# Kernel optimization log

Measured on AMD Instinct MI355X. Metric: run time of the kernel, lower is better.

Reference implementation:

```python
import jax, jax.numpy as jnp
import numpy as np

NF = 64            # n_filter
CFAC = 3           # SinSobel c_factor: identity + sobel-x + sobel-y
FIN = NF * CFAC    # dyna block input channels (192)
FH = NF * 2        # dyna hidden (128)
FOUT = NF          # dyna output (64)
LAT = 512
N_CALLS = 6        # ceil(log2(128) - log2(2))
P_SIZES = [FH * FIN, FH, FH * FH, FH, FOUT * FH, FOUT, FOUT * FIN, FOUT]
P_TOTAL = sum(P_SIZES)  # 61824
_OFFS = np.cumsum([0] + P_SIZES)

def act(t):
    return jax.nn.leaky_relu(t, 0.2)

def conv1x1(x, w, b):
    # x [B,I,H,W], w [O,I] -> [B,O,H,W]
    return jnp.einsum('bihw,oi->bohw', x, w) + b[None, :, None, None]

def res_block(x, w0, b0, w1, b1):
    # GAN-stability style residual block with 1x1 convs
    return x + 0.1 * conv1x1(act(conv1x1(act(x), w0, b0)), w1, b1)

def depthwise3x3(x, k2d):
    C = x.shape[1]
    k = jnp.broadcast_to(k2d.astype(x.dtype), (C, 1, 3, 3))
    return jax.lax.conv_general_dilated(
        x, k, (1, 1), [(1, 1), (1, 1)],
        dimension_numbers=('NCHW', 'OIHW', 'NCHW'),
        feature_group_count=C)

SOBEL_X = jnp.array([[1., 0., -1.], [2., 0., -2.], [1., 0., -1.]], jnp.float32) / 8.0
SOBEL_Y = SOBEL_X.T
_g = jnp.exp(-0.5 * jnp.array([-1., 0., 1.], jnp.float32) ** 2)
GAUSS = jnp.outer(_g, _g)
GAUSS = GAUSS / GAUSS.sum()

def sin_sobel(x):
    return jnp.concatenate([x, depthwise3x3(x, SOBEL_X), depthwise3x3(x, SOBEL_Y)], axis=1)

def dyna_residual(x, params):
    # per-sample hypernetwork-generated 1x1-conv residual block
    B = x.shape[0]
    def take(i, shape):
        return params[:, _OFFS[i]:_OFFS[i + 1]].reshape((B,) + shape)
    w_in, b_in = take(0, (FH, FIN)), take(1, (FH,))
    w_mid, b_mid = take(2, (FH, FH)), take(3, (FH,))
    w_out, b_out = take(4, (FOUT, FH)), take(5, (FOUT,))
    w_sk, b_sk = take(6, (FOUT, FIN)), take(7, (FOUT,))
    def pconv(h, w, b):  # batched per-sample 1x1 conv
        return jnp.einsum('bihw,boi->bohw', h, w) + b[:, :, None, None]
    x_s = pconv(x, w_sk, b_sk)
    dx = pconv(x, w_in, b_in)
    dx = pconv(act(dx), w_mid, b_mid)
    dx = pconv(act(dx), w_out, b_out)
    return x_s + dx

def downsample(x):
    # GaussianSmoothing(k=3, sigma=1, pad=1) then bilinear 0.5
    # (align_corners=False bilinear at scale 0.5 == 2x2 average pooling)
    x = depthwise3x3(x, GAUSS)
    B, C, H, W = x.shape
    return x.reshape(B, C, H // 2, 2, W // 2, 2).mean(axis=(3, 5))

def lin_res(x, w1, b1, w2, b2, sw=None, sb=None):
    x_s = x if sw is None else x @ sw + sb
    return x_s + 0.1 * (act(act(x) @ w1 + b1) @ w2 + b2)

def forward(x, inj_lat, leak, in_w, in_b, inrb_w0, inrb_b0, inrb_w1, inrb_b1,
            hyp_w, hyp_b, outrb_w0, outrb_b0, outrb_w1, outrb_b1,
            l1_sw, l1_sb, l1_w1, l1_b1, l1_w2, l1_b2,
            l2_w1, l2_b1, l2_w2, l2_b2, lo_w, lo_b):
    out = conv1x1(x, in_w, in_b)
    out = res_block(out, inrb_w0, inrb_b0, inrb_w1, inrb_b1)
    leak_f = jnp.clip(leak, 0.001, 1000.0)
    dyn_params = inj_lat @ hyp_w + hyp_b  # [B, P_TOTAL], shared across calls
    out_embs = [out]
    for _ in range(N_CALLS):  # fixed small layer loop; spatial dims halve each call
        out_new = sin_sobel(out)
        out_new = dyna_residual(out_new, dyn_params)
        out = out + leak_f * out_new
        out = downsample(out)
        out_embs.append(out)
    out = res_block(out, outrb_w0, outrb_b0, outrb_w1, outrb_b1)
    h = out.mean(axis=(2, 3))  # [B, NF]
    h = lin_res(h, l1_w1, l1_b1, l1_w2, l1_b2, l1_sw, l1_sb)
    h = lin_res(h, l2_w1, l2_b1, l2_w2, l2_b2)
    lat = h @ lo_w + lo_b
    return lat, out_embs

def setup_inputs() -> dict:
    key = jax.random.key(0)
    ks = jax.random.split(key, 24)
    B, C, S = 8, 3, 128
    def rn(k, shape, scale=0.05):
        return scale * jax.random.normal(k, shape, jnp.float32)
    z = lambda n: jnp.zeros((n,), jnp.float32)
    return {
        'x': jax.random.normal(ks[0], (B, C, S, S), jnp.float32),
        'inj_lat': jax.random.normal(ks[1], (B, LAT), jnp.float32),
        'leak': jnp.array(0.1, jnp.float32),
        'in_w': rn(ks[2], (NF, C)), 'in_b': z(NF),
        'inrb_w0': rn(ks[3], (NF, NF)), 'inrb_b0': z(NF),
        'inrb_w1': rn(ks[4], (NF, NF)), 'inrb_b1': z(NF),
        'hyp_w': rn(ks[5], (LAT, P_TOTAL), 0.01), 'hyp_b': rn(ks[6], (P_TOTAL,), 0.01),
        'outrb_w0': rn(ks[7], (NF, NF)), 'outrb_b0': z(NF),
        'outrb_w1': rn(ks[8], (NF, NF)), 'outrb_b1': z(NF),
        'l1_sw': rn(ks[9], (NF, LAT)), 'l1_sb': z(LAT),
        'l1_w1': rn(ks[10], (NF, 2 * LAT)), 'l1_b1': z(2 * LAT),
        'l1_w2': rn(ks[11], (2 * LAT, LAT)), 'l1_b2': z(LAT),
        'l2_w1': rn(ks[12], (LAT, LAT)), 'l2_b1': z(LAT),
        'l2_w2': rn(ks[13], (LAT, LAT)), 'l2_b2': z(LAT),
        'lo_w': rn(ks[14], (LAT, LAT)), 'lo_b': z(LAT),
    }

def reference(x, inj_lat, leak, in_w, in_b, inrb_w0, inrb_b0, inrb_w1, inrb_b1,
              hyp_w, hyp_b, outrb_w0, outrb_b0, outrb_w1, outrb_b1,
              l1_sw, l1_sb, l1_w1, l1_b1, l1_w2, l1_b2,
              l2_w1, l2_b1, l2_w2, l2_b2, lo_w, lo_b):
    lat, out_embs = forward(x, inj_lat, leak, in_w, in_b, inrb_w0, inrb_b0, inrb_w1, inrb_b1,
                            hyp_w, hyp_b, outrb_w0, outrb_b0, outrb_w1, outrb_b1,
                            l1_sw, l1_sb, l1_w1, l1_b1, l1_w2, l1_b2,
                            l2_w1, l2_b1, l2_w2, l2_b2, lo_w, lo_b)
    return (lat, *out_embs)
```

## Files before the change

kernel.cpp:

```cpp
#include <hip/hip_runtime.h>


#define BATCH 8
#define PT 61824

typedef __attribute__((ext_vector_type(8))) short bf16x8;
typedef __attribute__((ext_vector_type(4))) float f32x4;

__device__ __forceinline__ float lrelu(float v) { return v > 0.f ? v : 0.2f * v; }

__device__ __forceinline__ short f2bf(float f) {
    union { float fv; unsigned u; } v; v.fv = f;
    return (short)((v.u + 0x7fffu + ((v.u >> 16) & 1u)) >> 16);
}

__global__ __launch_bounds__(256) void hyper_kernel(
    const float* __restrict__ inj, const float* __restrict__ hw,
    const float* __restrict__ hb, float* __restrict__ dyn,
    short* __restrict__ dyn16)
{
    __shared__ float s_l[512 * 8];
    int t = threadIdx.x;
    for (int i = t; i < 4096; i += 256) {
        int b = i >> 9, k = i & 511;
        s_l[k * 8 + b] = inj[i];
    }
    __syncthreads();
    int p = blockIdx.x * 256 + t;
    if (p >= PT) return;
    float acc[8];
#pragma unroll
    for (int b = 0; b < 8; ++b) acc[b] = 0.f;
    for (int k = 0; k < 512; ++k) {
        float w = hw[(size_t)k * PT + p];
        float4 a0 = *(const float4*)&s_l[k * 8];
        float4 a1 = *(const float4*)&s_l[k * 8 + 4];
        acc[0] += a0.x * w; acc[1] += a0.y * w; acc[2] += a0.z * w; acc[3] += a0.w * w;
        acc[4] += a1.x * w; acc[5] += a1.y * w; acc[6] += a1.z * w; acc[7] += a1.w * w;
    }
    float bias = hb[p];
#pragma unroll
    for (int b = 0; b < 8; ++b) {
        float v = acc[b] + bias;
        dyn[(size_t)b * PT + p] = v;
        dyn16[(size_t)b * PT + p] = f2bf(v);
    }
}

__global__ __launch_bounds__(256) void stem_kernel(
    const float* __restrict__ x, const float* __restrict__ in_w,
    const float* __restrict__ in_b,
    const float* __restrict__ w0, const float* __restrict__ b0,
    const float* __restrict__ w1, const float* __restrict__ b1,
    float* __restrict__ out0)
{
    const int HW = 128 * 128;
    __shared__ float s_t0[64 * 68];
    __shared__ float s_v[64 * 68];
    const int tilesPer = HW / 64;
    const int b = blockIdx.x / tilesPer;
    const int tile = blockIdx.x - b * tilesPer;
    const int pix0 = tile * 64;
    const int t = threadIdx.x;

    for (int job = t; job < 64 * 64; job += 256) {
        int p = job & 63, c = job >> 6;
        const float* xb = x + (size_t)b * 3 * HW + pix0 + p;
        float v = in_b[c] + xb[0] * in_w[c * 3] + xb[HW] * in_w[c * 3 + 1]
                + xb[2 * HW] * in_w[c * 3 + 2];
        s_t0[p * 68 + c] = v;
        s_v[p * 68 + c] = lrelu(v);
    }
    __syncthreads();

    const int o = t & 63, g = t >> 6;
    {
        float acc[16];
#pragma unroll
        for (int p = 0; p < 16; ++p) acc[p] = 0.f;
        const float* wr = w0 + o * 64;
        for (int k4 = 0; k4 < 16; ++k4) {
            float4 wv = ((const float4*)wr)[k4];
#pragma unroll
            for (int p = 0; p < 16; ++p) {
                float4 uv = *(const float4*)&s_v[(g * 16 + p) * 68 + k4 * 4];
                acc[p] += wv.x * uv.x + wv.y * uv.y + wv.z * uv.z + wv.w * uv.w;
            }
        }
        __syncthreads();
        float bi = b0[o];
#pragma unroll
        for (int p = 0; p < 16; ++p) s_v[(g * 16 + p) * 68 + o] = lrelu(acc[p] + bi);
    }
    __syncthreads();
    {
        float acc[16];
#pragma unroll
        for (int p = 0; p < 16; ++p) acc[p] = 0.f;
        const float* wr = w1 + o * 64;
        for (int k4 = 0; k4 < 16; ++k4) {
            float4 wv = ((const float4*)wr)[k4];
#pragma unroll
            for (int p = 0; p < 16; ++p) {
                float4 uv = *(const float4*)&s_v[(g * 16 + p) * 68 + k4 * 4];
                acc[p] += wv.x * uv.x + wv.y * uv.y + wv.z * uv.z + wv.w * uv.w;
            }
        }
        float bi = b1[o];
        float* ob = out0 + ((size_t)b * 64 + o) * HW;
#pragma unroll
        for (int p = 0; p < 16; ++p) {
            int pix = pix0 + g * 16 + p;
            ob[pix] = s_t0[(g * 16 + p) * 68 + o] + 0.1f * (acc[p] + bi);
        }
    }
}

template<int MT>
__global__ __launch_bounds__(256) void iter_kernel(
    const float* __restrict__ cur, const float* __restrict__ dynf,
    const short* __restrict__ dynb, const float* __restrict__ leak_p,
    float* __restrict__ y, int S, int sh)
{
    constexpr int PX = MT * 16;
    constexpr int SY = (MT == 4) ? 68 : 20;
    __shared__ short s_s[PX * 200];
    __shared__ short s_h[PX * 136];
    float* s_y = (float*)s_s;

    const int HW = S * S;
    const int tilesPer = HW / PX;
    const int b = blockIdx.x / tilesPer;
    const int tile = blockIdx.x - b * tilesPer;
    const int pix0 = tile * PX;
    const int t = threadIdx.x;
    const int l = t & 63, w = t >> 6;
    const int lp = l & 15, lq = l >> 4;
    const float* base = cur + (size_t)b * 64 * HW;

    {
        const int p = (MT == 4) ? (lp + 16 * w) : lp;
        const int gpx = pix0 + p;
        const int row = gpx >> sh;
        const int x = gpx & (S - 1);
        const bool rm = (row > 0), rp = (row < S - 1);
        const bool le = (lp == 0) && (x > 0);
        const bool re = (lp == 15) && (x < S - 1);
        const int iters = (MT == 4) ? 8 : 2;
        int* s32 = (int*)s_s;
        for (int i = 0; i < iters; ++i) {
            const int cp = (MT == 4) ? (lq + 4 * i) : (lq + 4 * w + 16 * i);
            unsigned pk_id = 0, pk_sx = 0, pk_sy = 0;
#pragma unroll
            for (int cc = 0; cc < 2; ++cc) {
                const int c = 2 * cp + cc;
                const float* ch = base + (size_t)c * HW + row * S;
                float vm = rm ? ch[x - S] : 0.f;
                float v0 = ch[x];
                float vp = rp ? ch[x + S] : 0.f;
                float elm = 0.f, el0 = 0.f, elp = 0.f, erm = 0.f, er0 = 0.f, erp = 0.f;
                if (le) { elm = rm ? ch[x - 1 - S] : 0.f; el0 = ch[x - 1]; elp = rp ? ch[x - 1 + S] : 0.f; }
                if (re) { erm = rm ? ch[x + 1 - S] : 0.f; er0 = ch[x + 1]; erp = rp ? ch[x + 1 + S] : 0.f; }
                float Lm = __shfl(vm, l - 1), L0 = __shfl(v0, l - 1), Lp = __shfl(vp, l - 1);
                float Rm = __shfl(vm, l + 1), R0 = __shfl(v0, l + 1), Rp = __shfl(vp, l + 1);
                if (lp == 0)  { Lm = elm; L0 = el0; Lp = elp; }
                if (lp == 15) { Rm = erm; R0 = er0; Rp = erp; }
                if (x == 0)     { Lm = 0.f; L0 = 0.f; Lp = 0.f; }
                if (x == S - 1) { Rm = 0.f; R0 = 0.f; Rp = 0.f; }
                float sx = (Lm - Rm + 2.f * (L0 - R0) + Lp - Rp) * 0.125f;
                float sy = (Lm + 2.f * vm + Rm - Lp - 2.f * vp - Rp) * 0.125f;
                unsigned hid = (unsigned short)f2bf(v0);
                unsigned hsx = (unsigned short)f2bf(sx);
                unsigned hsy = (unsigned short)f2bf(sy);
                pk_id |= hid << (16 * cc);
                pk_sx |= hsx << (16 * cc);
                pk_sy |= hsy << (16 * cc);
            }
            s32[p * 100 + cp] = (int)pk_id;
            s32[p * 100 + 32 + cp] = (int)pk_sx;
            s32[p * 100 + 64 + cp] = (int)pk_sy;
        }
    }
    __syncthreads();

    const short* wb = dynb + (size_t)b * PT;
    const float* pf = dynf + (size_t)b * PT;
    const f32x4 z4 = {0.f, 0.f, 0.f, 0.f};

    {
        f32x4 acc[2][MT];
#pragma unroll
        for (int n = 0; n < 2; ++n)
#pragma unroll
            for (int mt = 0; mt < MT; ++mt) acc[n][mt] = z4;
        for (int k = 0; k < 6; ++k) {
            bf16x8 a[MT];
#pragma unroll
            for (int mt = 0; mt < MT; ++mt)
                a[mt] = *(const bf16x8*)&s_s[(mt * 16 + lp) * 200 + k * 32 + lq * 8];
#pragma unroll
            for (int n = 0; n < 2; ++n) {
                int o = (w * 2 + n) * 16 + lp;
                bf16x8 bb = *(const bf16x8*)&wb[o * 192 + k * 32 + lq * 8];
#pragma unroll
                for (int mt = 0; mt < MT; ++mt)
                    acc[n][mt] = __builtin_amdgcn_mfma_f32_16x16x32_bf16(a[mt], bb, acc[n][mt], 0, 0, 0);
            }
        }
#pragma unroll
        for (int n = 0; n < 2; ++n) {
            int o = (w * 2 + n) * 16 + lp;
            float bi = pf[24576 + o];
#pragma unroll
            for (int mt = 0; mt < MT; ++mt)
#pragma unroll
                for (int r = 0; r < 4; ++r)
                    s_h[(mt * 16 + lq * 4 + r) * 136 + o] = f2bf(lrelu(acc[n][mt][r] + bi));
        }
    }
    __syncthreads();

    {
        f32x4 acc[2][MT];
#pragma unroll
        for (int n = 0; n < 2; ++n)
#pragma unroll
            for (int mt = 0; mt < MT; ++mt) acc[n][mt] = z4;
        for (int k = 0; k < 4; ++k) {
            bf16x8 a[MT];
#pragma unroll
            for (int mt = 0; mt < MT; ++mt)
                a[mt] = *(const bf16x8*)&s_h[(mt * 16 + lp) * 136 + k * 32 + lq * 8];
#pragma unroll
            for (int n = 0; n < 2; ++n) {
                int o = (w * 2 + n) * 16 + lp;
                bf16x8 bb = *(const bf16x8*)&wb[24704 + o * 128 + k * 32 + lq * 8];
#pragma unroll
                for (int mt = 0; mt < MT; ++mt)
                    acc[n][mt] = __builtin_amdgcn_mfma_f32_16x16x32_bf16(a[mt], bb, acc[n][mt], 0, 0, 0);
            }
        }
        __syncthreads();
#pragma unroll
        for (int n = 0; n < 2; ++n) {
            int o = (w * 2 + n) * 16 + lp;
            float bi = pf[41088 + o];
#pragma unroll
            for (int mt = 0; mt < MT; ++mt)
#pragma unroll
                for (int r = 0; r < 4; ++r)
                    s_h[(mt * 16 + lq * 4 + r) * 136 + o] = f2bf(lrelu(acc[n][mt][r] + bi));
        }
    }
    __syncthreads();

    {
        f32x4 acc[MT];
#pragma unroll
        for (int mt = 0; mt < MT; ++mt) acc[mt] = z4;
        int o = w * 16 + lp;
        for (int k = 0; k < 4; ++k) {
            bf16x8 bb = *(const bf16x8*)&wb[41216 + o * 128 + k * 32 + lq * 8];
#pragma unroll
            for (int mt = 0; mt < MT; ++mt) {
                bf16x8 a = *(const bf16x8*)&s_h[(mt * 16 + lp) * 136 + k * 32 + lq * 8];
                acc[mt] = __builtin_amdgcn_mfma_f32_16x16x32_bf16(a, bb, acc[mt], 0, 0, 0);
            }
        }
        for (int k = 0; k < 6; ++k) {
            bf16x8 bb = *(const bf16x8*)&wb[49472 + o * 192 + k * 32 + lq * 8];
#pragma unroll
            for (int mt = 0; mt < MT; ++mt) {
                bf16x8 a = *(const bf16x8*)&s_s[(mt * 16 + lp) * 200 + k * 32 + lq * 8];
                acc[mt] = __builtin_amdgcn_mfma_f32_16x16x32_bf16(a, bb, acc[mt], 0, 0, 0);
            }
        }
        float bi = pf[49408 + o] + pf[61760 + o];
        __syncthreads();
#pragma unroll
        for (int mt = 0; mt < MT; ++mt)
#pragma unroll
            for (int r = 0; r < 4; ++r)
                s_y[o * SY + mt * 16 + lq * 4 + r] = acc[mt][r] + bi;
    }
    __syncthreads();

    {
        float lk = fminf(fmaxf(leak_p[0], 0.001f), 1000.f);
        if (MT == 4) {
#pragma unroll
            for (int v = 0; v < 4; ++v) {
                int idx = v * 1024 + t * 4;
                int o = idx >> 6, px = idx & 63;
                f32x4 sv = *(const f32x4*)&s_y[o * SY + px];
                const float* cb = cur + ((size_t)b * 64 + o) * HW + pix0 + px;
                float* yb = y + ((size_t)b * 64 + o) * HW + pix0 + px;
                f32x4 cv = *(const f32x4*)cb;
                *(f32x4*)yb = cv + lk * sv;
            }
        } else {
            int o = t >> 2, px = (t & 3) * 4;
            f32x4 sv = *(const f32x4*)&s_y[o * SY + px];
            const float* cb = cur + ((size_t)b * 64 + o) * HW + pix0 + px;
            float* yb = y + ((size_t)b * 64 + o) * HW + pix0 + px;
            f32x4 cv = *(const f32x4*)cb;
            *(f32x4*)yb = cv + lk * sv;
        }
    }
}

__global__ __launch_bounds__(256) void down_kernel(
    const float* __restrict__ yin, float* __restrict__ outp, int S, int total)
{
    int idx = blockIdx.x * 256 + threadIdx.x;
    if (idx >= total) return;
    const float ga = 0.60653065971263342f;
    const float gs = 1.f / ((1.f + 2.f * ga) * (1.f + 2.f * ga));
    float g1[3] = {ga, 1.f, ga};
    int S2 = S >> 1;
    int ox = idx % S2;
    int r = idx / S2;
    int oy = r % S2;
    int bc = r / S2;
    const float* src = yin + (size_t)bc * S * S;
    float acc = 0.f;
#pragma unroll
    for (int py = 0; py < 2; ++py)
#pragma unroll
        for (int px = 0; px < 2; ++px) {
            int cy = 2 * oy + py, cx = 2 * ox + px;
#pragma unroll
            for (int dy = 0; dy < 3; ++dy) {
                int ay = cy + dy - 1;
                if (ay < 0 || ay >= S) continue;
#pragma unroll
                for (int dx = 0; dx < 3; ++dx) {
                    int ax = cx + dx - 1;
                    if (ax < 0 || ax >= S) continue;
                    acc += g1[dy] * g1[dx] * src[ay * S + ax];
                }
            }
        }
    outp[idx] = acc * 0.25f * gs;
}

__global__ __launch_bounds__(256) void head_a_kernel(
    const float* __restrict__ emb6,
    const float* __restrict__ w0, const float* __restrict__ b0,
    const float* __restrict__ w1, const float* __restrict__ b1,
    float* __restrict__ h)
{
    __shared__ float sm_t[256], sm_v[256], sm_r[256];
    int b = blockIdx.x, t = threadIdx.x;
    sm_t[t] = emb6[b * 256 + t];
    __syncthreads();
    {
        int o = t & 63, p = t >> 6;
        float acc = 0.f;
        for (int k = 0; k < 64; ++k) acc += w0[o * 64 + k] * lrelu(sm_t[k * 4 + p]);
        sm_v[o * 4 + p] = lrelu(acc + b0[o]);
    }
    __syncthreads();
    {
        int o = t & 63, p = t >> 6;
        float acc = 0.f;
        for (int k = 0; k < 64; ++k) acc += w1[o * 64 + k] * sm_v[k * 4 + p];
        sm_r[o * 4 + p] = sm_t[o * 4 + p] + 0.1f * (acc + b1[o]);
    }
    __syncthreads();
    if (t < 64)
        h[b * 64 + t] = 0.25f * (sm_r[t * 4] + sm_r[t * 4 + 1] + sm_r[t * 4 + 2] + sm_r[t * 4 + 3]);
}

__global__ __launch_bounds__(256) void head_b_kernel(
    const float* __restrict__ h, const float* __restrict__ w,
    const float* __restrict__ bias, float* __restrict__ t1)
{
    __shared__ float s_h[64];
    int id = blockIdx.x * 256 + threadIdx.x;
    int b = id >> 10, o = id & 1023;
    if (threadIdx.x < 64) s_h[threadIdx.x] = lrelu(h[b * 64 + threadIdx.x]);
    __syncthreads();
    float acc = 0.f;
    for (int k = 0; k < 64; ++k) acc += s_h[k] * w[k * 1024 + o];
    t1[b * 1024 + o] = lrelu(acc + bias[o]);
}

__global__ __launch_bounds__(256) void head_c_kernel(
    const float* __restrict__ h, const float* __restrict__ t1,
    const float* __restrict__ sw, const float* __restrict__ sb,
    const float* __restrict__ w2, const float* __restrict__ b2,
    float* __restrict__ h1)
{
    __shared__ float s_t[8 * 128];
    __shared__ float s_h[8 * 64];
    int oblk = blockIdx.x & 1, chunk = blockIdx.x >> 1;
    int t = threadIdx.x;
    int o = oblk * 256 + t;
    for (int j = t; j < 1024; j += 256) {
        int b = j >> 7, kk = j & 127;
        s_t[j] = t1[b * 1024 + chunk * 128 + kk];
    }
    if (chunk == 0)
        for (int j = t; j < 512; j += 256) s_h[j] = h[j];
    __syncthreads();
    float acc[8];
#pragma unroll
    for (int b = 0; b < 8; ++b) acc[b] = 0.f;
    for (int kk = 0; kk < 128; ++kk) {
        float wv = w2[(chunk * 128 + kk) * 512 + o];
#pragma unroll
        for (int b = 0; b < 8; ++b) acc[b] += s_t[b * 128 + kk] * wv;
    }
#pragma unroll
    for (int b = 0; b < 8; ++b) acc[b] *= 0.1f;
    if (chunk == 0) {
        for (int k = 0; k < 64; ++k) {
            float wv = sw[k * 512 + o];
#pragma unroll
            for (int b = 0; b < 8; ++b) acc[b] += s_h[b * 64 + k] * wv;
        }
        float c0 = sb[o] + 0.1f * b2[o];
#pragma unroll
        for (int b = 0; b < 8; ++b) acc[b] += c0;
    }
#pragma unroll
    for (int b = 0; b < 8; ++b) atomicAdd(&h1[b * 512 + o], acc[b]);
}

__global__ __launch_bounds__(256) void head_d_kernel(
    const float* __restrict__ h1, const float* __restrict__ w,
    const float* __restrict__ bias, float* __restrict__ z3)
{
    __shared__ float s_u[8 * 64];
    int oblk = blockIdx.x & 1, chunk = blockIdx.x >> 1;
    int t = threadIdx.x;
    int o = oblk * 256 + t;
    for (int j = t; j < 512; j += 256) {
        int b = j >> 6, kk = j & 63;
        s_u[j] = lrelu(h1[b * 512 + chunk * 64 + kk]);
    }
    __syncthreads();
    float acc[8];
#pragma unroll
    for (int b = 0; b < 8; ++b) acc[b] = 0.f;
    for (int kk = 0; kk < 64; ++kk) {
        float wv = w[(chunk * 64 + kk) * 512 + o];
#pragma unroll
        for (int b = 0; b < 8; ++b) acc[b] += s_u[b * 64 + kk] * wv;
    }
    if (chunk == 0) {
        float c0 = bias[o];
#pragma unroll
        for (int b = 0; b < 8; ++b) acc[b] += c0;
    }
#pragma unroll
    for (int b = 0; b < 8; ++b) atomicAdd(&z3[b * 512 + o], acc[b]);
}

__global__ __launch_bounds__(256) void head_e_kernel(
    const float* __restrict__ h1, const float* __restrict__ z3,
    const float* __restrict__ w, const float* __restrict__ bias,
    float* __restrict__ h2)
{
    __shared__ float s_u[8 * 64];
    int oblk = blockIdx.x & 1, chunk = blockIdx.x >> 1;
    int t = threadIdx.x;
    int o = oblk * 256 + t;
    for (int j = t; j < 512; j += 256) {
        int b = j >> 6, kk = j & 63;
        s_u[j] = lrelu(z3[b * 512 + chunk * 64 + kk]);
    }
    __syncthreads();
    float acc[8];
#pragma unroll
    for (int b = 0; b < 8; ++b) acc[b] = 0.f;
    for (int kk = 0; kk < 64; ++kk) {
        float wv = w[(chunk * 64 + kk) * 512 + o];
#pragma unroll
        for (int b = 0; b < 8; ++b) acc[b] += s_u[b * 64 + kk] * wv;
    }
#pragma unroll
    for (int b = 0; b < 8; ++b) acc[b] *= 0.1f;
    if (chunk == 0) {
        float c0 = 0.1f * bias[o];
#pragma unroll
        for (int b = 0; b < 8; ++b) acc[b] += h1[b * 512 + o] + c0;
    }
#pragma unroll
    for (int b = 0; b < 8; ++b) atomicAdd(&h2[b * 512 + o], acc[b]);
}

__global__ __launch_bounds__(256) void head_f_kernel(
    const float* __restrict__ h2, const float* __restrict__ w,
    const float* __restrict__ bias, float* __restrict__ lat)
{
    __shared__ float s_u[8 * 64];
    int oblk = blockIdx.x & 1, chunk = blockIdx.x >> 1;
    int t = threadIdx.x;
    int o = oblk * 256 + t;
    for (int j = t; j < 512; j += 256) {
        int b = j >> 6, kk = j & 63;
        s_u[j] = h2[b * 512 + chunk * 64 + kk];
    }
    __syncthreads();
    float acc[8];
#pragma unroll
    for (int b = 0; b < 8; ++b) acc[b] = 0.f;
    for (int kk = 0; kk < 64; ++kk) {
        float wv = w[(chunk * 64 + kk) * 512 + o];
#pragma unroll
        for (int b = 0; b < 8; ++b) acc[b] += s_u[b * 64 + kk] * wv;
    }
    if (chunk == 0) {
        float c0 = bias[o];
#pragma unroll
        for (int b = 0; b < 8; ++b) acc[b] += c0;
    }
#pragma unroll
    for (int b = 0; b < 8; ++b) atomicAdd(&lat[b * 512 + o], acc[b]);
}

extern "C" void kernel_launch(void* const* d_in, const int* in_sizes, int n_in,
                              void* d_out, int out_size, void* d_ws, size_t ws_size,
                              hipStream_t stream) {
    const float* x      = (const float*)d_in[0];
    const float* inj    = (const float*)d_in[1];
    const float* leak   = (const float*)d_in[2];
    const float* in_w   = (const float*)d_in[3];
    const float* in_b   = (const float*)d_in[4];
    const float* inrb_w0 = (const float*)d_in[5];
    const float* inrb_b0 = (const float*)d_in[6];
    const float* inrb_w1 = (const float*)d_in[7];
    const float* inrb_b1 = (const float*)d_in[8];
    const float* hyp_w  = (const float*)d_in[9];
    const float* hyp_b  = (const float*)d_in[10];
    const float* outrb_w0 = (const float*)d_in[11];
    const float* outrb_b0 = (const float*)d_in[12];
    const float* outrb_w1 = (const float*)d_in[13];
    const float* outrb_b1 = (const float*)d_in[14];
    const float* l1_sw  = (const float*)d_in[15];
    const float* l1_sb  = (const float*)d_in[16];
    const float* l1_w1  = (const float*)d_in[17];
    const float* l1_b1  = (const float*)d_in[18];
    const float* l1_w2  = (const float*)d_in[19];
    const float* l1_b2  = (const float*)d_in[20];
    const float* l2_w1  = (const float*)d_in[21];
    const float* l2_b1  = (const float*)d_in[22];
    const float* l2_w2  = (const float*)d_in[23];
    const float* l2_b2  = (const float*)d_in[24];
    const float* lo_w   = (const float*)d_in[25];
    const float* lo_b   = (const float*)d_in[26];

    float* out = (float*)d_out;
    float* dyn = (float*)d_ws;
    float* ybuf = dyn + (size_t)BATCH * PT;
    short* dyn16 = (short*)(ybuf + (size_t)BATCH * 64 * 16384);
    float* hbuf = (float*)(dyn16 + (size_t)BATCH * PT);
    float* t1buf = hbuf + 512;
    float* h1buf = t1buf + 8192;
    float* z3buf = h1buf + 4096;
    float* h2buf = z3buf + 4096;

    hipMemsetAsync(h1buf, 0, (4096 * 3) * sizeof(float), stream);
    hipMemsetAsync(out, 0, 4096 * sizeof(float), stream);

    hyper_kernel<<<(PT + 255) / 256, 256, 0, stream>>>(inj, hyp_w, hyp_b, dyn, dyn16);

    size_t cur = 4096;
    stem_kernel<<<BATCH * 256, 256, 0, stream>>>(
        x, in_w, in_b, inrb_w0, inrb_b0, inrb_w1, inrb_b1, out + cur);

    int S = 128, sh = 7;
    for (int i = 0; i < 6; ++i) {
        if (S >= 64) {
            iter_kernel<4><<<BATCH * (S * S / 64), 256, 0, stream>>>(
                out + cur, dyn, dyn16, leak, ybuf, S, sh);
        } else {
            iter_kernel<1><<<BATCH * (S * S / 16), 256, 0, stream>>>(
                out + cur, dyn, dyn16, leak, ybuf, S, sh);
        }
        int S2 = S >> 1;
        int total = BATCH * 64 * S2 * S2;
        size_t nxt = cur + (size_t)BATCH * 64 * S * S;
        down_kernel<<<(total + 255) / 256, 256, 0, stream>>>(ybuf, out + nxt, S, total);
        cur = nxt;
        S = S2; sh -= 1;
    }

    head_a_kernel<<<BATCH, 256, 0, stream>>>(
        out + cur, outrb_w0, outrb_b0, outrb_w1, outrb_b1, hbuf);
    head_b_kernel<<<32, 256, 0, stream>>>(hbuf, l1_w1, l1_b1, t1buf);
    head_c_kernel<<<16, 256, 0, stream>>>(hbuf, t1buf, l1_sw, l1_sb, l1_w2, l1_b2, h1buf);
    head_d_kernel<<<16, 256, 0, stream>>>(h1buf, l2_w1, l2_b1, z3buf);
    head_e_kernel<<<16, 256, 0, stream>>>(h1buf, z3buf, l2_w2, l2_b2, h2buf);
    head_f_kernel<<<16, 256, 0, stream>>>(h2buf, lo_w, lo_b, out);
}
```

Before: 577.1 us.

## Fuse MLP head kernels into one persistent kernel with grid barriers

Replaces the six small head kernels and two memsets with a single 16-block kernel that steps through the MLP stages, separated by a software grid barrier on an atomic counter that down_kernel resets. Atomic split-K accumulation gives way to direct writes, with each block owning output columns and staging activations in shared memory. The goal is to remove launch and memset overhead on the tail of the program. It depends on all 16 blocks being resident at once, and the head now runs on few blocks with long serial K loops. The bf16 rounding also changes from round-to-nearest-even to round-half-up.

```diff
diff --git a/kernel.cpp b/kernel.cpp
--- a/kernel.cpp
+++ b/kernel.cpp
@@ -3,6 +3,7 @@
 
 #define BATCH 8
 #define PT 61824
+#define HNB 16
 
 typedef __attribute__((ext_vector_type(8))) short bf16x8;
 typedef __attribute__((ext_vector_type(4))) float f32x4;
@@ -11,7 +12,20 @@
 
 __device__ __forceinline__ short f2bf(float f) {
     union { float fv; unsigned u; } v; v.fv = f;
-    return (short)((v.u + 0x7fffu + ((v.u >> 16) & 1u)) >> 16);
+    return (short)((v.u + 0x8000u) >> 16);
+}
+
+__device__ __forceinline__ void grid_barrier(int* bar, int gen) {
+    __threadfence();
+    __syncthreads();
+    if (threadIdx.x == 0) {
+        atomicAdd(bar, 1);
+        int target = gen * HNB;
+        while (__hip_atomic_load(bar, __ATOMIC_RELAXED, __HIP_MEMORY_SCOPE_AGENT) < target)
+            __builtin_amdgcn_s_sleep(1);
+        __threadfence();
+    }
+    __syncthreads();
 }
 
 __global__ __launch_bounds__(256) void hyper_kernel(
@@ -310,9 +324,11 @@
 }
 
 __global__ __launch_bounds__(256) void down_kernel(
-    const float* __restrict__ yin, float* __restrict__ outp, int S, int total)
+    const float* __restrict__ yin, float* __restrict__ outp, int S, int total,
+    int* __restrict__ bar)
 {
     int idx = blockIdx.x * 256 + threadIdx.x;
+    if (idx == 0) *bar = 0;
     if (idx >= total) return;
     const float ga = 0.60653065971263342f;
     const float gs = 1.f / ((1.f + 2.f * ga) * (1.f + 2.f * ga));
@@ -344,181 +360,113 @@
     outp[idx] = acc * 0.25f * gs;
 }
 
-__global__ __launch_bounds__(256) void head_a_kernel(
+__global__ __launch_bounds__(256) void head_kernel(
     const float* __restrict__ emb6,
     const float* __restrict__ w0, const float* __restrict__ b0,
     const float* __restrict__ w1, const float* __restrict__ b1,
-    float* __restrict__ h)
+    const float* __restrict__ l1_sw, const float* __restrict__ l1_sb,
+    const float* __restrict__ l1_w1, const float* __restrict__ l1_b1,
+    const float* __restrict__ l1_w2, const float* __restrict__ l1_b2,
+    const float* __restrict__ l2_w1, const float* __restrict__ l2_b1,
+    const float* __restrict__ l2_w2, const float* __restrict__ l2_b2,
+    const float* __restrict__ lo_w, const float* __restrict__ lo_b,
+    float* __restrict__ hbuf, float* __restrict__ t1buf,
+    float* __restrict__ h1buf, float* __restrict__ t3buf,
+    float* __restrict__ h2buf, int* __restrict__ bar,
+    float* __restrict__ lat)
 {
-    __shared__ float sm_t[256], sm_v[256], sm_r[256];
-    int b = blockIdx.x, t = threadIdx.x;
-    sm_t[t] = emb6[b * 256 + t];
-    __syncthreads();
-    {
-        int o = t & 63, p = t >> 6;
+    __shared__ float smem[8192 + 512];
+    const int bk = blockIdx.x, t = threadIdx.x;
+
+    if (bk < 8) {
+        float* sm_t = smem;
+        float* sm_v = smem + 256;
+        float* sm_r = smem + 512;
+        sm_t[t] = emb6[bk * 256 + t];
+        __syncthreads();
+        {
+            int o = t & 63, p = t >> 6;
+            float a = 0.f;
+            for (int k = 0; k < 64; ++k) a += w0[o * 64 + k] * lrelu(sm_t[k * 4 + p]);
+            sm_v[o * 4 + p] = lrelu(a + b0[o]);
+        }
+        __syncthreads();
+        {
+            int o = t & 63, p = t >> 6;
+            float a = 0.f;
+            for (int k = 0; k < 64; ++k) a += w1[o * 64 + k] * sm_v[k * 4 + p];
+            sm_r[o * 4 + p] = sm_t[o * 4 + p] + 0.1f * (a + b1[o]);
+        }
+        __syncthreads();
+        if (t < 64)
+            hbuf[bk * 64 + t] = 0.25f * (sm_r[t * 4] + sm_r[t * 4 + 1] + sm_r[t * 4 + 2] + sm_r[t * 4 + 3]);
+    }
+    grid_barrier(bar, 1);
+
+    {
+        float* s_h = smem;
+        for (int j = t; j < 512; j += 256) s_h[j] = lrelu(hbuf[j]);
+        __syncthreads();
+        int col = bk * 64 + (t & 63);
+        int b4 = t >> 6;
+        float a0 = 0.f, a1 = 0.f;
+        for (int k = 0; k < 64; ++k) {
+            float wv = l1_w1[k * 1024 + col];
+            a0 += s_h[b4 * 64 + k] * wv;
+            a1 += s_h[(b4 + 4) * 64 + k] * wv;
+        }
+        float bi = l1_b1[col];
+        t1buf[b4 * 1024 + col] = lrelu(a0 + bi);
+        t1buf[(b4 + 4) * 1024 + col] = lrelu(a1 + bi);
+    }
+    grid_barrier(bar, 2);
+
+    {
+        float* s_t1 = smem;
+        float* s_hr = smem + 8192;
+        for (int j = t; j < 8192; j += 256) s_t1[j] = t1buf[j];
+        for (int j = t; j < 512; j += 256) s_hr[j] = hbuf[j];
+        __syncthreads();
+        int gcol = bk * 32 + (t & 31), b = t >> 5;
         float acc = 0.f;
-        for (int k = 0; k < 64; ++k) acc += w0[o * 64 + k] * lrelu(sm_t[k * 4 + p]);
-        sm_v[o * 4 + p] = lrelu(acc + b0[o]);
-    }
-    __syncthreads();
-    {
-        int o = t & 63, p = t >> 6;
+        for (int k = 0; k < 1024; ++k) acc += s_t1[b * 1024 + k] * l1_w2[k * 512 + gcol];
+        float accs = 0.f;
+        for (int k = 0; k < 64; ++k) accs += s_hr[b * 64 + k] * l1_sw[k * 512 + gcol];
+        h1buf[b * 512 + gcol] = accs + l1_sb[gcol] + 0.1f * (acc + l1_b2[gcol]);
+    }
+    grid_barrier(bar, 3);
+
+    {
+        float* s_u = smem;
+        for (int j = t; j < 4096; j += 256) s_u[j] = lrelu(h1buf[j]);
+        __syncthreads();
+        int gcol = bk * 32 + (t & 31), b = t >> 5;
         float acc = 0.f;
-        for (int k = 0; k < 64; ++k) acc += w1[o * 64 + k] * sm_v[k * 4 + p];
-        sm_r[o * 4 + p] = sm_t[o * 4 + p] + 0.1f * (acc + b1[o]);
-    }
-    __syncthreads();
-    if (t < 64)
-        h[b * 64 + t] = 0.25f * (sm_r[t * 4] + sm_r[t * 4 + 1] + sm_r[t * 4 + 2] + sm_r[t * 4 + 3]);
-}
-
-__global__ __launch_bounds__(256) void head_b_kernel(
-    const float* __restrict__ h, const float* __restrict__ w,
-    const float* __restrict__ bias, float* __restrict__ t1)
-{
-    __shared__ float s_h[64];
-    int id = blockIdx.x * 256 + threadIdx.x;
-    int b = id >> 10, o = id & 1023;
-    if (threadIdx.x < 64) s_h[threadIdx.x] = lrelu(h[b * 64 + threadIdx.x]);
-    __syncthreads();
-    float acc = 0.f;
-    for (int k = 0; k < 64; ++k) acc += s_h[k] * w[k * 1024 + o];
-    t1[b * 1024 + o] = lrelu(acc + bias[o]);
-}
-
-__global__ __launch_bounds__(256) void head_c_kernel(
-    const float* __restrict__ h, const float* __restrict__ t1,
-    const float* __restrict__ sw, const float* __restrict__ sb,
-    const float* __restrict__ w2, const float* __restrict__ b2,
-    float* __restrict__ h1)
-{
-    __shared__ float s_t[8 * 128];
-    __shared__ float s_h[8 * 64];
-    int oblk = blockIdx.x & 1, chunk = blockIdx.x >> 1;
-    int t = threadIdx.x;
-    int o = oblk * 256 + t;
-    for (int j = t; j < 1024; j += 256) {
-        int b = j >> 7, kk = j & 127;
-        s_t[j] = t1[b * 1024 + chunk * 128 + kk];
-    }
-    if (chunk == 0)
-        for (int j = t; j < 512; j += 256) s_h[j] = h[j];
-    __syncthreads();
-    float acc[8];
-#pragma unroll
-    for (int b = 0; b < 8; ++b) acc[b] = 0.f;
-    for (int kk = 0; kk < 128; ++kk) {
-        float wv = w2[(chunk * 128 + kk) * 512 + o];
-#pragma unroll
-        for (int b = 0; b < 8; ++b) acc[b] += s_t[b * 128 + kk] * wv;
-    }
-#pragma unroll
-    for (int b = 0; b < 8; ++b) acc[b] *= 0.1f;
-    if (chunk == 0) {
-        for (int k = 0; k < 64; ++k) {
-            float wv = sw[k * 512 + o];
-#pragma unroll
-            for (int b = 0; b < 8; ++b) acc[b] += s_h[b * 64 + k] * wv;
-        }
-        float c0 = sb[o] + 0.1f * b2[o];
-#pragma unroll
-        for (int b = 0; b < 8; ++b) acc[b] += c0;
-    }
-#pragma unroll
-    for (int b = 0; b < 8; ++b) atomicAdd(&h1[b * 512 + o], acc[b]);
-}
-
-__global__ __launch_bounds__(256) void head_d_kernel(
-    const float* __restrict__ h1, const float* __restrict__ w,
-    const float* __restrict__ bias, float* __restrict__ z3)
-{
-    __shared__ float s_u[8 * 64];
-    int oblk = blockIdx.x & 1, chunk = blockIdx.x >> 1;
-    int t = threadIdx.x;
-    int o = oblk * 256 + t;
-    for (int j = t; j < 512; j += 256) {
-        int b = j >> 6, kk = j & 63;
-        s_u[j] = lrelu(h1[b * 512 + chunk * 64 + kk]);
-    }
-    __syncthreads();
-    float acc[8];
-#pragma unroll
-    for (int b = 0; b < 8; ++b) acc[b] = 0.f;
-    for (int kk = 0; kk < 64; ++kk) {
-        float wv = w[(chunk * 64 + kk) * 512 + o];
-#pragma unroll
-        for (int b = 0; b < 8; ++b) acc[b] += s_u[b * 64 + kk] * wv;
-    }
-    if (chunk == 0) {
-        float c0 = bias[o];
-#pragma unroll
-        for (int b = 0; b < 8; ++b) acc[b] += c0;
-    }
-#pragma unroll
-    for (int b = 0; b < 8; ++b) atomicAdd(&z3[b * 512 + o], acc[b]);
-}
-
-__global__ __launch_bounds__(256) void head_e_kernel(
-    const float* __restrict__ h1, const float* __restrict__ z3,
-    const float* __restrict__ w, const float* __restrict__ bias,
-    float* __restrict__ h2)
-{
-    __shared__ float s_u[8 * 64];
-    int oblk = blockIdx.x & 1, chunk = blockIdx.x >> 1;
-    int t = threadIdx.x;
-    int o = oblk * 256 + t;
-    for (int j = t; j < 512; j += 256) {
-        int b = j >> 6, kk = j & 63;
-        s_u[j] = lrelu(z3[b * 512 + chunk * 64 + kk]);
-    }
-    __syncthreads();
-    float acc[8];
-#pragma unroll
-    for (int b = 0; b < 8; ++b) acc[b] = 0.f;
-    for (int kk = 0; kk < 64; ++kk) {
-        float wv = w[(chunk * 64 + kk) * 512 + o];
-#pragma unroll
-        for (int b = 0; b < 8; ++b) acc[b] += s_u[b * 64 + kk] * wv;
-    }
-#pragma unroll
-    for (int b = 0; b < 8; ++b) acc[b] *= 0.1f;
-    if (chunk == 0) {
-        float c0 = 0.1f * bias[o];
-#pragma unroll
-        for (int b = 0; b < 8; ++b) acc[b] += h1[b * 512 + o] + c0;
-    }
-#pragma unroll
-    for (int b = 0; b < 8; ++b) atomicAdd(&h2[b * 512 + o], acc[b]);
-}
-
-__global__ __launch_bounds__(256) void head_f_kernel(
-    const float* __restrict__ h2, const float* __restrict__ w,
-    const float* __restrict__ bias, float* __restrict__ lat)
-{
-    __shared__ float s_u[8 * 64];
-    int oblk = blockIdx.x & 1, chunk = blockIdx.x >> 1;
-    int t = threadIdx.x;
-    int o = oblk * 256 + t;
-    for (int j = t; j < 512; j += 256) {
-        int b = j >> 6, kk = j & 63;
-        s_u[j] = h2[b * 512 + chunk * 64 + kk];
-    }
-    __syncthreads();
-    float acc[8];
-#pragma unroll
-    for (int b = 0; b < 8; ++b) acc[b] = 0.f;
-    for (int kk = 0; kk < 64; ++kk) {
-        float wv = w[(chunk * 64 + kk) * 512 + o];
-#pragma unroll
-        for (int b = 0; b < 8; ++b) acc[b] += s_u[b * 64 + kk] * wv;
-    }
-    if (chunk == 0) {
-        float c0 = bias[o];
-#pragma unroll
-        for (int b = 0; b < 8; ++b) acc[b] += c0;
-    }
-#pragma unroll
-    for (int b = 0; b < 8; ++b) atomicAdd(&lat[b * 512 + o], acc[b]);
+        for (int k = 0; k < 512; ++k) acc += s_u[b * 512 + k] * l2_w1[k * 512 + gcol];
+        t3buf[b * 512 + gcol] = lrelu(acc + l2_b1[gcol]);
+    }
+    grid_barrier(bar, 4);
+
+    {
+        float* s_u = smem;
+        for (int j = t; j < 4096; j += 256) s_u[j] = t3buf[j];
+        __syncthreads();
+        int gcol = bk * 32 + (t & 31), b = t >> 5;
+        float acc = 0.f;
+        for (int k = 0; k < 512; ++k) acc += s_u[b * 512 + k] * l2_w2[k * 512 + gcol];
+        h2buf[b * 512 + gcol] = h1buf[b * 512 + gcol] + 0.1f * (acc + l2_b2[gcol]);
+    }
+    grid_barrier(bar, 5);
+
+    {
+        float* s_u = smem;
+        for (int j = t; j < 4096; j += 256) s_u[j] = h2buf[j];
+        __syncthreads();
+        int gcol = bk * 32 + (t & 31), b = t >> 5;
+        float acc = 0.f;
+        for (int k = 0; k < 512; ++k) acc += s_u[b * 512 + k] * lo_w[k * 512 + gcol];
+        lat[b * 512 + gcol] = acc + lo_b[gcol];
+    }
 }
 
 extern "C" void kernel_launch(void* const* d_in, const int* in_sizes, int n_in,
@@ -559,11 +507,9 @@
     float* hbuf = (float*)(dyn16 + (size_t)BATCH * PT);
     float* t1buf = hbuf + 512;
     float* h1buf = t1buf + 8192;
-    float* z3buf = h1buf + 4096;
-    float* h2buf = z3buf + 4096;
-
-    hipMemsetAsync(h1buf, 0, (4096 * 3) * sizeof(float), stream);
-    hipMemsetAsync(out, 0, 4096 * sizeof(float), stream);
+    float* t3buf = h1buf + 4096;
+    float* h2buf = t3buf + 4096;
+    int* bar = (int*)(h2buf + 4096);
 
     hyper_kernel<<<(PT + 255) / 256, 256, 0, stream>>>(inj, hyp_w, hyp_b, dyn, dyn16);
 
@@ -583,16 +529,14 @@
         int S2 = S >> 1;
         int total = BATCH * 64 * S2 * S2;
         size_t nxt = cur + (size_t)BATCH * 64 * S * S;
-        down_kernel<<<(total + 255) / 256, 256, 0, stream>>>(ybuf, out + nxt, S, total);
+        down_kernel<<<(total + 255) / 256, 256, 0, stream>>>(ybuf, out + nxt, S, total, bar);
         cur = nxt;
         S = S2; sh -= 1;
     }
 
-    head_a_kernel<<<BATCH, 256, 0, stream>>>(
-        out + cur, outrb_w0, outrb_b0, outrb_w1, outrb_b1, hbuf);
-    head_b_kernel<<<32, 256, 0, stream>>>(hbuf, l1_w1, l1_b1, t1buf);
-    head_c_kernel<<<16, 256, 0, stream>>>(hbuf, t1buf, l1_sw, l1_sb, l1_w2, l1_b2, h1buf);
-    head_d_kernel<<<16, 256, 0, stream>>>(h1buf, l2_w1, l2_b1, z3buf);
-    head_e_kernel<<<16, 256, 0, stream>>>(h1buf, z3buf, l2_w2, l2_b2, h2buf);
-    head_f_kernel<<<16, 256, 0, stream>>>(h2buf, lo_w, lo_b, out);
-}
+    head_kernel<<<HNB, 256, 0, stream>>>(
+        out + cur, outrb_w0, outrb_b0, outrb_w1, outrb_b1,
+        l1_sw, l1_sb, l1_w1, l1_b1, l1_w2, l1_b2,
+        l2_w1, l2_b1, l2_w2, l2_b2, lo_w, lo_b,
+        hbuf, t1buf, h1buf, t3buf, h2buf, bar, out);
+}
```

New measurement: 708.2 us. 1.23x slower.
